# Optimization experiments

Measured on AMD Instinct MI355X. Metric: run time of the kernel, lower is better.

The kernel has to match this reference:

```python
import jax, jax.numpy as jnp
import numpy as np

B, N, D, H = 2, 2048, 2048, 16
HD = D // H  # head_dim = 128
EPS = 1e-06

def rmsnorm(x, w, eps=EPS):
    xf = x.astype(jnp.float32)
    y = xf * jax.lax.rsqrt(jnp.mean(xf * xf, axis=-1, keepdims=True) + eps)
    return y.astype(x.dtype) * w

def rope_apply(x, freqs, num_heads):
    # x: [B, S, D]; freqs: [S, 1, HD//2, 2] = (cos, sin) of complex rotation
    b, s, d = x.shape
    hd = d // num_heads
    xr = x.reshape(b, s, num_heads, hd // 2, 2)
    x0, x1 = xr[..., 0], xr[..., 1]
    fr, fi = freqs[..., 0], freqs[..., 1]  # broadcast [S,1,HD//2] over heads
    out = jnp.stack([x0 * fr - x1 * fi, x0 * fi + x1 * fr], axis=-1)
    return out.reshape(b, s, d).astype(x.dtype)

def attention(q, k, v, num_heads):
    b, s, d = q.shape
    hd = d // num_heads
    qh = q.reshape(b, s, num_heads, hd).transpose(0, 2, 1, 3)  # b h s d
    kh = k.reshape(b, s, num_heads, hd).transpose(0, 2, 1, 3)
    vh = v.reshape(b, s, num_heads, hd).transpose(0, 2, 1, 3)
    scale = hd ** -0.5
    scores = jnp.einsum('bhqd,bhkd->bhqk', qh, kh) * scale
    probs = jax.nn.softmax(scores, axis=-1)
    out = jnp.einsum('bhqk,bhkd->bhqd', probs, vh)
    return out.transpose(0, 2, 1, 3).reshape(b, s, d)

def setup_inputs() -> dict:
    key = jax.random.key(0)
    ks = jax.random.split(key, 8)
    x = jax.random.normal(ks[0], (B, N, D), jnp.float32)
    # standard RoPE frequencies
    pos = jnp.arange(N, dtype=jnp.float32)
    inv = 1.0 / (10000.0 ** (jnp.arange(0, HD, 2, dtype=jnp.float32) / HD))
    ang = pos[:, None] * inv[None, :]  # [N, HD//2]
    freqs = jnp.stack([jnp.cos(ang), jnp.sin(ang)], axis=-1)[:, None, :, :]  # [N,1,HD//2,2]
    s = 0.02
    wq = jax.random.normal(ks[1], (D, D), jnp.float32) * s
    wk = jax.random.normal(ks[2], (D, D), jnp.float32) * s
    wv = jax.random.normal(ks[3], (D, D), jnp.float32) * s
    wo = jax.random.normal(ks[4], (D, D), jnp.float32) * s
    bq = jnp.zeros((D,), jnp.float32)
    bk = jnp.zeros((D,), jnp.float32)
    bv = jnp.zeros((D,), jnp.float32)
    bo = jnp.zeros((D,), jnp.float32)
    gq = jnp.ones((D,), jnp.float32)
    gk = jnp.ones((D,), jnp.float32)
    return {"x": x, "freqs": freqs, "wq": wq, "bq": bq, "wk": wk, "bk": bk,
            "wv": wv, "bv": bv, "wo": wo, "bo": bo, "gq": gq, "gk": gk}

def reference(x, freqs, wq, bq, wk, bk, wv, bv, wo, bo, gq, gk):
    q = rmsnorm(x @ wq.T + bq, gq)
    k = rmsnorm(x @ wk.T + bk, gk)
    v = x @ wv.T + bv
    q = rope_apply(q, freqs, H)
    k = rope_apply(k, freqs, H)
    attn_out = attention(q, k, v, H)
    return attn_out @ wo.T + bo
```

## Files before the change

kernel.cpp:

```cpp
#include <hip/hip_runtime.h>
#include <hip/hip_bf16.h>
#include <stdint.h>


typedef __bf16 bf16;
typedef __bf16 bf16x8 __attribute__((ext_vector_type(8)));
typedef __bf16 bf16x4 __attribute__((ext_vector_type(4)));
typedef float  f32x4  __attribute__((ext_vector_type(4)));
typedef float  f32x16 __attribute__((ext_vector_type(16)));
typedef unsigned int uint2v __attribute__((ext_vector_type(2)));

#define MTOT   4096
#define DMODEL 2048
#define NSEQ   2048
#define NHEAD  16
#define HDIM   128

static __device__ __forceinline__ void async_ld16(const void* g, void* l) {
  void* gnc = const_cast<void*>(g);
  __builtin_amdgcn_global_load_lds((__attribute__((address_space(1))) void*)gnc,
                                   (__attribute__((address_space(3))) void*)l,
                                   16, 0, 0);
}

static __device__ __forceinline__ float exp2_hw(float x) {
  float r;
  asm("v_exp_f32 %0, %1" : "=v"(r) : "v"(x));
  return r;
}

#define XG (MTOT * DMODEL / 8)
#define WG (DMODEL * DMODEL / 8)

__global__ __launch_bounds__(256) void k_cvt4(
    const float* __restrict__ x, const float* __restrict__ wq,
    const float* __restrict__ wk, const float* __restrict__ wv,
    bf16* __restrict__ xb, bf16* __restrict__ wqb, bf16* __restrict__ wkb,
    bf16* __restrict__ wvb) {
  int stride = gridDim.x * blockDim.x;
  for (int i = blockIdx.x * blockDim.x + threadIdx.x; i < XG + 3 * WG;
       i += stride) {
    const float* src;
    bf16* dst;
    int off;
    if (i < XG) { src = x; dst = xb; off = i; }
    else if (i < XG + WG) { src = wq; dst = wqb; off = i - XG; }
    else if (i < XG + 2 * WG) { src = wk; dst = wkb; off = i - XG - WG; }
    else { src = wv; dst = wvb; off = i - XG - 2 * WG; }
    const float4* p = (const float4*)(src) + 2 * (size_t)off;
    float4 a = p[0], b = p[1];
    bf16x8 o;
    o[0] = (bf16)a.x; o[1] = (bf16)a.y; o[2] = (bf16)a.z; o[3] = (bf16)a.w;
    o[4] = (bf16)b.x; o[5] = (bf16)b.y; o[6] = (bf16)b.z; o[7] = (bf16)b.w;
    *((bf16x8*)(dst) + off) = o;
  }
}

__global__ __launch_bounds__(256) void k_cvt(const float* __restrict__ in,
                                             bf16* __restrict__ out, int n8) {
  int stride = gridDim.x * blockDim.x;
  for (int i = blockIdx.x * blockDim.x + threadIdx.x; i < n8; i += stride) {
    const float4* p = (const float4*)(in) + 2 * (size_t)i;
    float4 a = p[0], b = p[1];
    bf16x8 o;
    o[0] = (bf16)a.x; o[1] = (bf16)a.y; o[2] = (bf16)a.z; o[3] = (bf16)a.w;
    o[4] = (bf16)b.x; o[5] = (bf16)b.y; o[6] = (bf16)b.z; o[7] = (bf16)b.w;
    *((bf16x8*)(out) + i) = o;
  }
}

__global__ __launch_bounds__(512, 2) void k_gemm_qk(
    const bf16* __restrict__ xb, const bf16* __restrict__ wq,
    const bf16* __restrict__ wk, const float* __restrict__ bq,
    const float* __restrict__ bk, bf16* __restrict__ q, bf16* __restrict__ k) {
  extern __shared__ __align__(16) bf16 dyn[];

  const int swz = (blockIdx.x & 7) * 32 + (blockIdx.x >> 3);
  const int mt = swz >> 4, nt = swz & 15;
  const int sec = nt >> 3;
  const int m0 = mt * 256, n0 = (nt & 7) * 256;
  const bf16* W = sec ? wk : wq;
  const float* bias = sec ? bk : bq;
  bf16* outp = sec ? k : q;

  const int tid = threadIdx.x;
  const int lane = tid & 63, w = tid >> 6;
  const int wm = w >> 2, wn = w & 3;
  const int g = lane >> 4, r0 = lane & 15;

  f32x4 acc[8][4];
  const f32x4 vzero = {0.f, 0.f, 0.f, 0.f};
#pragma unroll
  for (int i = 0; i < 8; ++i)
#pragma unroll
    for (int j = 0; j < 4; ++j) acc[i][j] = vzero;

  const bf16* Abase = xb + (size_t)m0 * DMODEL;
  const bf16* Wbase = W + (size_t)n0 * DMODEL;

  auto stage = [&](int kt, int buf) {
    const bf16* asrc = Abase + kt * 64;
    const bf16* bsrc = Wbase + kt * 64;
    bf16* sA = dyn + buf * 32768;
    bf16* sB = sA + 16384;
#pragma unroll
    for (int p = 0; p < 4; ++p) {
      int ch = tid + p * 512;
      int row = ch >> 3, c = (ch & 7) ^ (row & 7);
      async_ld16(asrc + (size_t)row * DMODEL + c * 8, sA + ch * 8);
    }
#pragma unroll
    for (int p = 0; p < 4; ++p) {
      int ch = tid + p * 512;
      int row = ch >> 3, c = (ch & 7) ^ (row & 7);
      async_ld16(bsrc + (size_t)row * DMODEL + c * 8, sB + ch * 8);
    }
  };

  const int NT = DMODEL / 64;
  stage(0, 0);
  for (int kt = 0; kt < NT; ++kt) {
    const int cur = kt & 1;
    if (kt > 0) __builtin_amdgcn_s_barrier();
    if (kt + 1 < NT) {
      stage(kt + 1, cur ^ 1);
      asm volatile("s_waitcnt vmcnt(8)" ::: "memory");
    } else {
      asm volatile("s_waitcnt vmcnt(0)" ::: "memory");
    }
    __builtin_amdgcn_s_barrier();
    const bf16* sA = dyn + cur * 32768;
    const bf16* sB = sA + 16384;

    bf16x8 a0[8], a1[8], b0[4], b1[4];
#pragma unroll
    for (int i = 0; i < 4; ++i) {
      int ra = wm * 128 + i * 16 + r0;
#pragma unroll
      for (int ks = 0; ks < 2; ++ks) {
        int cc = ks * 4 + g;
        a0[i * 2 + ks] = *(const bf16x8*)(sA + ra * 64 + ((cc ^ (ra & 7)) << 3));
      }
    }
#pragma unroll
    for (int j = 0; j < 2; ++j) {
      int rb = wn * 64 + j * 16 + r0;
#pragma unroll
      for (int ks = 0; ks < 2; ++ks) {
        int cc = ks * 4 + g;
        b0[j * 2 + ks] = *(const bf16x8*)(sB + rb * 64 + ((cc ^ (rb & 7)) << 3));
      }
    }
#pragma unroll
    for (int j = 0; j < 2; ++j) {
      int rb = wn * 64 + 32 + j * 16 + r0;
#pragma unroll
      for (int ks = 0; ks < 2; ++ks) {
        int cc = ks * 4 + g;
        b1[j * 2 + ks] = *(const bf16x8*)(sB + rb * 64 + ((cc ^ (rb & 7)) << 3));
      }
    }
    __builtin_amdgcn_s_setprio(1);
#pragma unroll
    for (int i = 0; i < 4; ++i)
#pragma unroll
      for (int j = 0; j < 2; ++j)
#pragma unroll
        for (int ks = 0; ks < 2; ++ks)
          acc[i][j] = __builtin_amdgcn_mfma_f32_16x16x32_bf16(
              a0[i * 2 + ks], b0[j * 2 + ks], acc[i][j], 0, 0, 0);
    __builtin_amdgcn_s_setprio(0);
#pragma unroll
    for (int i = 0; i < 4; ++i) {
      int ra = wm * 128 + 64 + i * 16 + r0;
#pragma unroll
      for (int ks = 0; ks < 2; ++ks) {
        int cc = ks * 4 + g;
        a1[i * 2 + ks] = *(const bf16x8*)(sA + ra * 64 + ((cc ^ (ra & 7)) << 3));
      }
    }
    __builtin_amdgcn_s_setprio(1);
#pragma unroll
    for (int i = 0; i < 4; ++i)
#pragma unroll
      for (int j = 0; j < 2; ++j)
#pragma unroll
        for (int ks = 0; ks < 2; ++ks)
          acc[i][2 + j] = __builtin_amdgcn_mfma_f32_16x16x32_bf16(
              a0[i * 2 + ks], b1[j * 2 + ks], acc[i][2 + j], 0, 0, 0);
    __builtin_amdgcn_s_setprio(0);
    __builtin_amdgcn_s_setprio(1);
#pragma unroll
    for (int i = 0; i < 4; ++i)
#pragma unroll
      for (int j = 0; j < 2; ++j)
#pragma unroll
        for (int ks = 0; ks < 2; ++ks)
          acc[4 + i][j] = __builtin_amdgcn_mfma_f32_16x16x32_bf16(
              a1[i * 2 + ks], b0[j * 2 + ks], acc[4 + i][j], 0, 0, 0);
    __builtin_amdgcn_s_setprio(0);
    __builtin_amdgcn_s_setprio(1);
#pragma unroll
    for (int i = 0; i < 4; ++i)
#pragma unroll
      for (int j = 0; j < 2; ++j)
#pragma unroll
        for (int ks = 0; ks < 2; ++ks)
          acc[4 + i][2 + j] = __builtin_amdgcn_mfma_f32_16x16x32_bf16(
              a1[i * 2 + ks], b1[j * 2 + ks], acc[4 + i][2 + j], 0, 0, 0);
    __builtin_amdgcn_s_setprio(0);
  }

#pragma unroll
  for (int i = 0; i < 8; ++i) {
#pragma unroll
    for (int j = 0; j < 4; ++j) {
      int mb = m0 + wm * 128 + (i >> 2) * 64 + (i & 3) * 16 + g * 4;
      int n = n0 + wn * 64 + (j >> 1) * 32 + (j & 1) * 16 + r0;
      float bn = bias[n];
#pragma unroll
      for (int r = 0; r < 4; ++r)
        outp[(size_t)(mb + r) * DMODEL + n] = (bf16)(acc[i][j][r] + bn);
    }
  }
}

#define BUFELEMS (384 * 64)

template <int OUTMODE>
static __device__ __forceinline__ void gemm256_body(
    const bf16* __restrict__ A, const bf16* __restrict__ W,
    const float* __restrict__ bias, void* __restrict__ outp, int m0, int n0) {
  extern __shared__ __align__(16) bf16 dynls[];

  const int tid = threadIdx.x;
  const int lane = tid & 63, w = tid >> 6;
  const int wm = w >> 2, wn = w & 3;
  const int g = lane >> 4, r0 = lane & 15;

  f32x4 acc[4][4];
  const f32x4 vzero = {0.f, 0.f, 0.f, 0.f};
#pragma unroll
  for (int i = 0; i < 4; ++i)
#pragma unroll
    for (int j = 0; j < 4; ++j) acc[i][j] = vzero;

  const bf16* Abase = A + (size_t)m0 * DMODEL;
  const bf16* Wbase = W + (size_t)n0 * DMODEL;

  auto stage_a = [&](int kt, int buf) {
    const bf16* asrc = Abase + kt * 64;
    const bf16* bsrc = Wbase + kt * 64;
    bf16* sBuf = dynls + buf * BUFELEMS;
#pragma unroll
    for (int p = 0; p < 2; ++p) {
      int ch = tid + p * 512;
      int row = ch >> 3, c = (ch & 7) ^ (row & 7);
      async_ld16(asrc + (size_t)row * DMODEL + c * 8, sBuf + ch * 8);
    }
    {
      int ch = tid;
      int row = ch >> 3, c = (ch & 7) ^ (row & 7);
      async_ld16(bsrc + (size_t)row * DMODEL + c * 8, sBuf + 128 * 64 + ch * 8);
    }
  };
  auto stage_b = [&](int kt, int buf) {
    const bf16* bsrc = Wbase + kt * 64;
    bf16* sBuf = dynls + buf * BUFELEMS + 128 * 64;
#pragma unroll
    for (int p = 1; p < 4; ++p) {
      int ch = tid + p * 512;
      int row = ch >> 3, c = (ch & 7) ^ (row & 7);
      async_ld16(bsrc + (size_t)row * DMODEL + c * 8, sBuf + ch * 8);
    }
  };

  const int NT = DMODEL / 64;
  stage_a(0, 0); stage_b(0, 0);
  stage_a(1, 1); stage_b(1, 1);
  asm volatile("s_waitcnt vmcnt(6)" ::: "memory");
  __builtin_amdgcn_s_barrier();

  for (int kt = 0; kt < NT; ++kt) {
    const bf16* sA = dynls + (kt % 3) * BUFELEMS;
    const bf16* sB = sA + 128 * 64;
    const bool pf = (kt + 2) < NT;
    const int nb = (kt + 2) % 3;

#pragma unroll
    for (int ks = 0; ks < 2; ++ks) {
      bf16x8 af[4], bfr[4];
      const int cc = ks * 4 + g;
#pragma unroll
      for (int i = 0; i < 4; ++i) {
        int ra = wm * 64 + i * 16 + r0;
        af[i] = *(const bf16x8*)(sA + ra * 64 + ((cc ^ (ra & 7)) << 3));
        int rb = wn * 64 + i * 16 + r0;
        bfr[i] = *(const bf16x8*)(sB + rb * 64 + ((cc ^ (rb & 7)) << 3));
      }
      if (ks == 0) {
        if (pf) stage_a(kt + 2, nb);
      } else {
        if (pf) {
          stage_b(kt + 2, nb);
          asm volatile("s_waitcnt vmcnt(6)" ::: "memory");
        } else {
          asm volatile("s_waitcnt vmcnt(0)" ::: "memory");
        }
      }
      __builtin_amdgcn_sched_barrier(0);
      __builtin_amdgcn_s_barrier();
      __builtin_amdgcn_sched_barrier(0);
      __builtin_amdgcn_s_setprio(1);
#pragma unroll
      for (int i = 0; i < 4; ++i)
#pragma unroll
        for (int j = 0; j < 4; ++j)
          acc[i][j] = __builtin_amdgcn_mfma_f32_16x16x32_bf16(af[i], bfr[j],
                                                              acc[i][j], 0, 0, 0);
      __builtin_amdgcn_s_setprio(0);
    }
  }

#pragma unroll
  for (int i = 0; i < 4; ++i) {
#pragma unroll
    for (int j = 0; j < 4; ++j) {
      int mb = m0 + wm * 64 + i * 16 + g * 4;
      int n = n0 + wn * 64 + j * 16 + r0;
      float bn = bias[n];
      if (OUTMODE == 0) {
        bf16* o = (bf16*)outp;
#pragma unroll
        for (int r = 0; r < 4; ++r)
          o[(size_t)(mb + r) * DMODEL + n] = (bf16)(acc[i][j][r] + bn);
      } else if (OUTMODE == 2) {
        float* o = (float*)outp;
#pragma unroll
        for (int r = 0; r < 4; ++r)
          o[(size_t)(mb + r) * DMODEL + n] = acc[i][j][r] + bn;
      } else {
        bf16* o = (bf16*)outp;
        int bb = mb >> 11, s = mb & (NSEQ - 1);
        bf16x4 pk;
#pragma unroll
        for (int r = 0; r < 4; ++r) pk[r] = (bf16)(acc[i][j][r] + bn);
        *(bf16x4*)(o + (size_t)(bb * DMODEL + n) * NSEQ + s) = pk;
      }
    }
  }
}

__global__ __launch_bounds__(512, 2) void k_gemm_v(
    const bf16* __restrict__ xb, const bf16* __restrict__ wv,
    const float* __restrict__ bv, bf16* __restrict__ vt) {
  gemm256_body<1>(xb, wv, bv, vt, blockIdx.y * 128, blockIdx.x * 256);
}

__global__ __launch_bounds__(512, 2) void k_gemm_out(
    const bf16* __restrict__ ab, const bf16* __restrict__ wo,
    const float* __restrict__ bo, float* __restrict__ out) {
  gemm256_body<2>(ab, wo, bo, out, blockIdx.y * 128, blockIdx.x * 256);
}

__global__ __launch_bounds__(256) void k_norm_rope(
    bf16* __restrict__ q, bf16* __restrict__ kk, const float* __restrict__ gq,
    const float* __restrict__ gk, const float* __restrict__ freqs) {
  int bidx = blockIdx.x;
  bf16* buf = (bidx < MTOT) ? q : kk;
  const float* gw = (bidx < MTOT) ? gq : gk;
  float qs = (bidx < MTOT) ? (0.08838834764831845f * 1.4426950408889634f)
                           : 1.0f;
  int row = bidx & (MTOT - 1);
  int s = row & (NSEQ - 1);
  int tid = threadIdx.x;
  int i0 = tid * 8;
  bf16* ptr = buf + (size_t)row * DMODEL + i0;
  bf16x8 v = *(const bf16x8*)ptr;
  float x[8];
  float ssq = 0.f;
#pragma unroll
  for (int j = 0; j < 8; ++j) {
    x[j] = (float)v[j];
    ssq += x[j] * x[j];
  }
#pragma unroll
  for (int off = 1; off < 64; off <<= 1) ssq += __shfl_xor(ssq, off);
  __shared__ float part[4];
  if ((tid & 63) == 0) part[tid >> 6] = ssq;
  __syncthreads();
  float tot = part[0] + part[1] + part[2] + part[3];
  float sc = rsqrtf(tot * (1.f / DMODEL) + 1e-6f) * qs;
  float4 g0 = *(const float4*)(gw + i0);
  float4 g1 = *(const float4*)(gw + i0 + 4);
  float y[8];
  y[0] = x[0] * sc * g0.x; y[1] = x[1] * sc * g0.y;
  y[2] = x[2] * sc * g0.z; y[3] = x[3] * sc * g0.w;
  y[4] = x[4] * sc * g1.x; y[5] = x[5] * sc * g1.y;
  y[6] = x[6] * sc * g1.z; y[7] = x[7] * sc * g1.w;
  int dl = i0 & (HDIM - 1);
  const float* fp = freqs + (size_t)s * HDIM + dl;
  float4 f0 = *(const float4*)fp;
  float4 f1 = *(const float4*)(fp + 4);
  bf16x8 out;
  out[0] = (bf16)(y[0] * f0.x - y[1] * f0.y);
  out[1] = (bf16)(y[0] * f0.y + y[1] * f0.x);
  out[2] = (bf16)(y[2] * f0.z - y[3] * f0.w);
  out[3] = (bf16)(y[2] * f0.w + y[3] * f0.z);
  out[4] = (bf16)(y[4] * f1.x - y[5] * f1.y);
  out[5] = (bf16)(y[4] * f1.y + y[5] * f1.x);
  out[6] = (bf16)(y[6] * f1.z - y[7] * f1.w);
  out[7] = (bf16)(y[6] * f1.w + y[7] * f1.z);
  *(bf16x8*)ptr = out;
}

#define LOG2E_THR 11.541560327111707f

__global__ __launch_bounds__(256, 2) void k_attn(const bf16* __restrict__ q,
                                                 const bf16* __restrict__ k,
                                                 const bf16* __restrict__ vt,
                                                 bf16* __restrict__ o) {
  __shared__ __align__(16) bf16 sk[2][64 * 128];
  __shared__ __align__(16) bf16 sv[2][128 * 64];
  const int bid = blockIdx.x;
  const int idx = bid >> 3;
  const int bh = (bid & 7) * 4 + (idx >> 4);
  const int qt = idx & 15;
  const int bb = bh >> 4, h = bh & 15;
  const int tid = threadIdx.x;
  const int lane = tid & 63, w = tid >> 6;
  const int l31 = lane & 31, b5 = lane >> 5;

  bf16x8 qf[8];
  {
    const bf16* qb =
        q + (size_t)(bb * NSEQ + qt * 128 + w * 32 + l31) * DMODEL + h * HDIM +
        b5 * 8;
#pragma unroll
    for (int kk = 0; kk < 8; ++kk) qf[kk] = *(const bf16x8*)(qb + kk * 16);
  }

  f32x16 oacc[4];
#pragma unroll
  for (int dt = 0; dt < 4; ++dt)
#pragma unroll
    for (int r = 0; r < 16; ++r) oacc[dt][r] = 0.f;
  float m = 0.f, l = 0.f;

  const bf16* kbase = k + (size_t)(bb * NSEQ) * DMODEL + h * HDIM;
  const bf16* vbase = vt + (size_t)(bb * DMODEL + h * HDIM) * NSEQ;

  auto stage = [&](int t, int buf) {
    int k0 = t * 64;
#pragma unroll
    for (int p = 0; p < 4; ++p) {
      int ch = tid + p * 256;
      int row = ch >> 4, cs = ch & 15;
      int c = cs ^ (row & 15);
      async_ld16(kbase + (size_t)(k0 + row) * DMODEL + c * 8, &sk[buf][ch * 8]);
    }
#pragma unroll
    for (int p = 0; p < 4; ++p) {
      int ch = tid + p * 256;
      int row = ch >> 3, cs = ch & 7;
      int c = cs ^ (row & 7);
      async_ld16(vbase + (size_t)row * NSEQ + k0 + c * 8, &sv[buf][ch * 8]);
    }
  };

  stage(0, 0);
  for (int t = 0; t < NSEQ / 64; ++t) {
    const int cur = t & 1;
    asm volatile("s_waitcnt vmcnt(0)" ::: "memory");
    __syncthreads();
    if (t + 1 < NSEQ / 64) stage(t + 1, cur ^ 1);

    f32x16 sacc[2];
#pragma unroll
    for (int s = 0; s < 2; ++s)
#pragma unroll
      for (int r = 0; r < 16; ++r) sacc[s][r] = -m;
    __builtin_amdgcn_s_setprio(1);
#pragma unroll
    for (int s = 0; s < 2; ++s) {
      const int row = s * 32 + l31;
#pragma unroll
      for (int kk = 0; kk < 8; ++kk) {
        const int c = 2 * kk + b5;
        bf16x8 kf = *(const bf16x8*)(&sk[cur][row * 128 + ((c ^ (row & 15)) << 3)]);
        sacc[s] = __builtin_amdgcn_mfma_f32_32x32x16_bf16(kf, qf[kk], sacc[s],
                                                          0, 0, 0);
      }
    }
    __builtin_amdgcn_s_setprio(0);

    float t1[8];
#pragma unroll
    for (int i = 0; i < 8; ++i)
      t1[i] = fmaxf(fmaxf(sacc[0][2 * i], sacc[0][2 * i + 1]),
                    fmaxf(sacc[1][2 * i], sacc[1][2 * i + 1]));
    float pm = fmaxf(fmaxf(fmaxf(t1[0], t1[1]), fmaxf(t1[2], t1[3])),
                     fmaxf(fmaxf(t1[4], t1[5]), fmaxf(t1[6], t1[7])));
    {
      uint2v r2 = __builtin_amdgcn_permlane32_swap(__float_as_uint(pm),
                                                   __float_as_uint(pm), false,
                                                   false);
      pm = fmaxf(__uint_as_float(r2.x), __uint_as_float(r2.y));
    }
    if (__any(pm > LOG2E_THR)) {
      float d = fmaxf(pm, 0.f);
      m += d;
      float alpha = exp2_hw(-d);
      l *= alpha;
#pragma unroll
      for (int dt = 0; dt < 4; ++dt)
#pragma unroll
        for (int r = 0; r < 16; ++r) oacc[dt][r] *= alpha;
#pragma unroll
      for (int s = 0; s < 2; ++s)
#pragma unroll
        for (int r = 0; r < 16; ++r) sacc[s][r] -= d;
    }

    float rs = 0.f;
#pragma unroll
    for (int s = 0; s < 2; ++s)
#pragma unroll
      for (int r = 0; r < 16; ++r) {
        float pv = exp2_hw(sacc[s][r]);
        sacc[s][r] = pv;
        rs += pv;
      }
    {
      uint2v r2 = __builtin_amdgcn_permlane32_swap(__float_as_uint(rs),
                                                   __float_as_uint(rs), false,
                                                   false);
      rs = __uint_as_float(r2.x) + __uint_as_float(r2.y);
    }
    l += rs;

    uint32_t P2[16];
#pragma unroll
    for (int s = 0; s < 2; ++s)
#pragma unroll
      for (int i = 0; i < 8; ++i)
        asm("v_cvt_pk_bf16_f32 %0, %1, %2"
            : "=v"(P2[s * 8 + i])
            : "v"(sacc[s][2 * i]), "v"(sacc[s][2 * i + 1]));

    __builtin_amdgcn_s_setprio(1);
#pragma unroll
    for (int s = 0; s < 2; ++s) {
#pragma unroll
      for (int u = 0; u < 2; ++u) {
        union { uint32_t uw[4]; bf16x8 v; } pb;
        uint2v ra = __builtin_amdgcn_permlane32_swap(P2[s * 8 + 4 * u],
                                                     P2[s * 8 + 4 * u + 2],
                                                     false, false);
        uint2v rb = __builtin_amdgcn_permlane32_swap(P2[s * 8 + 4 * u + 1],
                                                     P2[s * 8 + 4 * u + 3],
                                                     false, false);
        pb.uw[0] = ra.x;
        pb.uw[1] = rb.x;
        pb.uw[2] = ra.y;
        pb.uw[3] = rb.y;
        const int c = 4 * s + 2 * u + b5;
#pragma unroll
        for (int dt = 0; dt < 4; ++dt) {
          const int rv = dt * 32 + l31;
          bf16x8 vf =
              *(const bf16x8*)(&sv[cur][rv * 64 + ((c ^ (rv & 7)) << 3)]);
          oacc[dt] = __builtin_amdgcn_mfma_f32_32x32x16_bf16(vf, pb.v, oacc[dt],
                                                             0, 0, 0);
        }
      }
    }
    __builtin_amdgcn_s_setprio(0);
  }

  const float rl = 1.f / l;
  bf16* ob = o + (size_t)(bb * NSEQ + qt * 128 + w * 32 + l31) * DMODEL +
             h * HDIM;
#pragma unroll
  for (int dt = 0; dt < 4; ++dt) {
#pragma unroll
    for (int rg = 0; rg < 4; ++rg) {
      bf16x4 pk4;
#pragma unroll
      for (int e = 0; e < 4; ++e) pk4[e] = (bf16)(oacc[dt][rg * 4 + e] * rl);
      *(bf16x4*)(ob + dt * 32 + rg * 8 + b5 * 4) = pk4;
    }
  }
}

extern "C" void kernel_launch(void* const* d_in, const int* in_sizes, int n_in,
                              void* d_out, int out_size, void* d_ws,
                              size_t ws_size, hipStream_t stream) {
  (void)in_sizes; (void)n_in; (void)out_size; (void)ws_size;
  const float* x = (const float*)d_in[0];
  const float* freqs = (const float*)d_in[1];
  const float* wq = (const float*)d_in[2];
  const float* bq = (const float*)d_in[3];
  const float* wk = (const float*)d_in[4];
  const float* bk = (const float*)d_in[5];
  const float* wv = (const float*)d_in[6];
  const float* bv = (const float*)d_in[7];
  const float* wo = (const float*)d_in[8];
  const float* bo = (const float*)d_in[9];
  const float* gq = (const float*)d_in[10];
  const float* gk = (const float*)d_in[11];

  char* ws = (char*)d_ws;
  const size_t SZ_TOK = (size_t)MTOT * DMODEL * sizeof(bf16);
  const size_t SZ_W = (size_t)DMODEL * DMODEL * sizeof(bf16);
  bf16* xb = (bf16*)ws;
  bf16* qb = (bf16*)(ws + SZ_TOK);
  bf16* kb = (bf16*)(ws + 2 * SZ_TOK);
  bf16* vtb = (bf16*)(ws + 3 * SZ_TOK);
  bf16* wqb = (bf16*)(ws + 4 * SZ_TOK);
  bf16* wkb = (bf16*)(ws + 4 * SZ_TOK + SZ_W);
  bf16* wvb = (bf16*)(ws + 4 * SZ_TOK + 2 * SZ_W);

  const int LDSB = 3 * BUFELEMS * (int)sizeof(bf16);
  const int LDSQK = 2 * 32768 * (int)sizeof(bf16);
  hipFuncSetAttribute((const void*)k_gemm_qk,
                      hipFuncAttributeMaxDynamicSharedMemorySize, LDSQK);
  hipFuncSetAttribute((const void*)k_gemm_v,
                      hipFuncAttributeMaxDynamicSharedMemorySize, LDSB);
  hipFuncSetAttribute((const void*)k_gemm_out,
                      hipFuncAttributeMaxDynamicSharedMemorySize, LDSB);

  k_cvt4<<<2048, 256, 0, stream>>>(x, wq, wk, wv, xb, wqb, wkb, wvb);

  k_gemm_qk<<<256, 512, LDSQK, stream>>>(xb, wqb, wkb, bq, bk, qb, kb);
  k_gemm_v<<<dim3(8, 32), 512, LDSB, stream>>>(xb, wvb, bv, vtb);

  k_cvt<<<1024, 256, 0, stream>>>(wo, wqb, (DMODEL * DMODEL) / 8);

  k_norm_rope<<<2 * MTOT, 256, 0, stream>>>(qb, kb, gq, gk, freqs);

  k_attn<<<512, 256, 0, stream>>>(qb, kb, vtb, xb);

  k_gemm_out<<<dim3(8, 32), 512, LDSB, stream>>>(xb, wqb, bo, (float*)d_out);
}
```

Baseline: 258.1 us.

## Compute softmax row sums with MFMA against ones and reswizzle V tile

Replaces the scalar row-sum accumulation and permlane reduction of softmax probabilities with an extra MFMA per P fragment that multiplies by a vector of ones into a dedicated accumulator. The V tile in shared memory is re-laid out as 64 rows of 128 with a 16-way XOR swizzle so the V reads can avoid bank conflicts. The max reduction is also restructured into a chained form. The sum now uses bf16-rounded probabilities, which matches the values fed to the PV product, and adds MFMA work plus 16 accumulator registers.

```diff
diff --git a/kernel.cpp b/kernel.cpp
--- a/kernel.cpp
+++ b/kernel.cpp
@@ -421,7 +421,7 @@
                                                  const bf16* __restrict__ vt,
                                                  bf16* __restrict__ o) {
   __shared__ __align__(16) bf16 sk[2][64 * 128];
-  __shared__ __align__(16) bf16 sv[2][128 * 64];
+  __shared__ __align__(16) bf16 sv[2][64 * 128];
   const int bid = blockIdx.x;
   const int idx = bid >> 3;
   const int bh = (bid & 7) * 4 + (idx >> 4);
@@ -445,7 +445,13 @@
   for (int dt = 0; dt < 4; ++dt)
 #pragma unroll
     for (int r = 0; r < 16; ++r) oacc[dt][r] = 0.f;
-  float m = 0.f, l = 0.f;
+  f32x16 sum_acc;
+#pragma unroll
+  for (int r = 0; r < 16; ++r) sum_acc[r] = 0.f;
+  float m = 0.f;
+
+  union { uint32_t u[4]; bf16x8 v; } ones;
+  ones.u[0] = ones.u[1] = ones.u[2] = ones.u[3] = 0x3F803F80u;
 
   const bf16* kbase = k + (size_t)(bb * NSEQ) * DMODEL + h * HDIM;
   const bf16* vbase = vt + (size_t)(bb * DMODEL + h * HDIM) * NSEQ;
@@ -462,9 +468,11 @@
 #pragma unroll
     for (int p = 0; p < 4; ++p) {
       int ch = tid + p * 256;
-      int row = ch >> 3, cs = ch & 7;
-      int c = cs ^ (row & 7);
-      async_ld16(vbase + (size_t)row * NSEQ + k0 + c * 8, &sv[buf][ch * 8]);
+      int r2 = ch >> 4, pos = ch & 15;
+      int idxv = pos ^ (r2 & 15);
+      int d = ((idxv >> 3) << 6) | r2;
+      int creal = idxv & 7;
+      async_ld16(vbase + (size_t)d * NSEQ + k0 + creal * 8, &sv[buf][ch * 8]);
     }
   };
 
@@ -496,11 +504,15 @@
 
     float t1[8];
 #pragma unroll
-    for (int i = 0; i < 8; ++i)
+    for (int i = 0; i < 8; ++i) {
       t1[i] = fmaxf(fmaxf(sacc[0][2 * i], sacc[0][2 * i + 1]),
-                    fmaxf(sacc[1][2 * i], sacc[1][2 * i + 1]));
-    float pm = fmaxf(fmaxf(fmaxf(t1[0], t1[1]), fmaxf(t1[2], t1[3])),
-                     fmaxf(fmaxf(t1[4], t1[5]), fmaxf(t1[6], t1[7])));
+                    sacc[1][2 * i]);
+      t1[i] = fmaxf(t1[i], sacc[1][2 * i + 1]);
+    }
+    float pm = fmaxf(fmaxf(t1[0], t1[1]), t1[2]);
+    pm = fmaxf(fmaxf(pm, t1[3]), t1[4]);
+    pm = fmaxf(fmaxf(pm, t1[5]), t1[6]);
+    pm = fmaxf(pm, t1[7]);
     {
       uint2v r2 = __builtin_amdgcn_permlane32_swap(__float_as_uint(pm),
                                                    __float_as_uint(pm), false,
@@ -511,7 +523,8 @@
       float d = fmaxf(pm, 0.f);
       m += d;
       float alpha = exp2_hw(-d);
-      l *= alpha;
+#pragma unroll
+      for (int r = 0; r < 16; ++r) sum_acc[r] *= alpha;
 #pragma unroll
       for (int dt = 0; dt < 4; ++dt)
 #pragma unroll
@@ -522,22 +535,10 @@
         for (int r = 0; r < 16; ++r) sacc[s][r] -= d;
     }
 
-    float rs = 0.f;
 #pragma unroll
     for (int s = 0; s < 2; ++s)
 #pragma unroll
-      for (int r = 0; r < 16; ++r) {
-        float pv = exp2_hw(sacc[s][r]);
-        sacc[s][r] = pv;
-        rs += pv;
-      }
-    {
-      uint2v r2 = __builtin_amdgcn_permlane32_swap(__float_as_uint(rs),
-                                                   __float_as_uint(rs), false,
-                                                   false);
-      rs = __uint_as_float(r2.x) + __uint_as_float(r2.y);
-    }
-    l += rs;
+      for (int r = 0; r < 16; ++r) sacc[s][r] = exp2_hw(sacc[s][r]);
 
     uint32_t P2[16];
 #pragma unroll
@@ -565,11 +566,14 @@
         pb.uw[2] = ra.y;
         pb.uw[3] = rb.y;
         const int c = 4 * s + 2 * u + b5;
+        sum_acc = __builtin_amdgcn_mfma_f32_32x32x16_bf16(ones.v, pb.v,
+                                                          sum_acc, 0, 0, 0);
 #pragma unroll
         for (int dt = 0; dt < 4; ++dt) {
           const int rv = dt * 32 + l31;
-          bf16x8 vf =
-              *(const bf16x8*)(&sv[cur][rv * 64 + ((c ^ (rv & 7)) << 3)]);
+          const int r2v = rv & 63;
+          const int pos = (((rv >> 6) << 3) | c) ^ (r2v & 15);
+          bf16x8 vf = *(const bf16x8*)(&sv[cur][r2v * 128 + pos * 8]);
           oacc[dt] = __builtin_amdgcn_mfma_f32_32x32x16_bf16(vf, pb.v, oacc[dt],
                                                              0, 0, 0);
         }
@@ -578,7 +582,7 @@
     __builtin_amdgcn_s_setprio(0);
   }
 
-  const float rl = 1.f / l;
+  const float rl = 1.f / sum_acc[0];
   bf16* ob = o + (size_t)(bb * NSEQ + qt * 128 + w * 32 + l31) * DMODEL +
              h * HDIM;
 #pragma unroll
```

Result: no change. 257.6 us (-0.2%).
